# Performance work log

Hardware: AMD Instinct MI355X
Metric: run time of the kernel (lower is better)

## Reference

```python
import jax, jax.numpy as jnp
import numpy as np

N, C_IN, T, V = 64, 64, 256, 25
S = 3            # num_subsets
C_OUT = 128
GROUPS = 8
EPS = 1e-5


def setup_inputs() -> dict:
    key = jax.random.key(0)
    ks = jax.random.split(key, 6)
    x = jax.random.normal(ks[0], (N, C_IN, T, V), dtype=jnp.float32)
    A = jax.random.uniform(ks[1], (S, V, V), dtype=jnp.float32) / V  # normalized-ish adjacency buffer
    PA = jax.random.normal(ks[2], (S, V, V), dtype=jnp.float32) * 0.01  # learnable adjacency offset
    cin_g = C_IN // GROUPS  # 8 input channels per group
    Wg = jax.random.normal(ks[3], (C_OUT * S, cin_g), dtype=jnp.float32) * (1.0 / np.sqrt(cin_g))
    bg = jax.random.normal(ks[4], (C_OUT * S,), dtype=jnp.float32) * 0.01
    gamma = jnp.ones((C_OUT,), dtype=jnp.float32)
    beta = jnp.zeros((C_OUT,), dtype=jnp.float32)
    return {"x": x, "A": A, "PA": PA, "Wg": Wg, "bg": bg, "gamma": gamma, "beta": beta}


def reference(x, A, PA, Wg, bg, gamma, beta):
    n, c, t, v = x.shape
    cin_g = c // GROUPS
    cout_total = Wg.shape[0]          # C_OUT * S
    cout_g = cout_total // GROUPS
    # grouped 1x1 conv: conv_group
    xg = x.reshape(n, GROUPS, cin_g, t, v)
    Wg_ = Wg.reshape(GROUPS, cout_g, cin_g)
    out = jnp.einsum('ngctv,gdc->ngdtv', xg, Wg_).reshape(n, cout_total, t, v)
    out = out + bg[None, :, None, None]
    # split into subsets and apply per-subset adjacency, accumulate
    outs = out.reshape(n, S, cout_total // S, t, v)   # (N,S,Cout,T,V)
    Aeff = A + PA                                      # (S,V,V)
    total = jnp.einsum('nsctv,svw->nctw', outs, Aeff)  # (N,Cout,T,V)
    # BatchNorm2d (training-mode batch statistics, biased variance)
    mean = total.mean(axis=(0, 2, 3), keepdims=True)
    var = ((total - mean) ** 2).mean(axis=(0, 2, 3), keepdims=True)
    y = (total - mean) * jax.lax.rsqrt(var + EPS)
    return y * gamma[None, :, None, None] + beta[None, :, None, None]
```

## Files before the change

kernel.cpp:

```cpp
#include <hip/hip_runtime.h>
#include <math.h>

#define NB   64
#define CIN  64
#define TDIM 256
#define VV   25
#define SS   3
#define COUT 128
#define NTV  (NB * TDIM * VV)
#define OUT_TOTAL (NB * COUT * TDIM * VV)
#define TT   8
#define NTILE (TDIM / TT)

#define WS_STATS 0
#define WS_AE2   2048
#define WS_W2    4160
#define WS_BIAS  7232
#define WS_SCALE 10816
#define WS_SHIFT 10944
#define MID_OFF  16384

__device__ __forceinline__ void fma4(float4& a, float s, const float4& b) {
    a.x = fmaf(s, b.x, a.x);
    a.y = fmaf(s, b.y, a.y);
    a.z = fmaf(s, b.z, a.z);
    a.w = fmaf(s, b.w, a.w);
}

__global__ void prep_kernel(const float* __restrict__ A, const float* __restrict__ PA,
                            const float* __restrict__ Wg, const float* __restrict__ bg,
                            float* __restrict__ ws) {
    const int tid = threadIdx.x;
    for (int i = tid; i < 2048; i += 256) ws[WS_STATS + i] = 0.0f;
    for (int i = tid; i < 25 * 84; i += 256) {
        int v = i / 84, r = i % 84;
        int s = r / 28, w = r % 28;
        float val = 0.0f;
        if (w < 25) {
            int idx = s * 625 + v * 25 + w;
            val = A[idx] + PA[idx];
        }
        ws[WS_AE2 + i] = val;
    }
    for (int i = tid; i < 24 * 128; i += 256) {
        int row = i / 128, c = i % 128;
        int s = row / 8, j = row % 8;
        ws[WS_W2 + i] = Wg[(s * 128 + c) * 8 + j];
    }
    for (int i = tid; i < 128 * 28; i += 256) {
        int c = i / 28, w = i % 28;
        float val = 0.0f;
        if (w < 25) {
            for (int s = 0; s < 3; ++s) {
                float cs = 0.0f;
                for (int v = 0; v < 25; ++v) {
                    int idx = s * 625 + v * 25 + w;
                    cs += A[idx] + PA[idx];
                }
                val += bg[s * 128 + c] * cs;
            }
        }
        ws[WS_BIAS + i] = val;
    }
}

template <bool PERM>
__global__ __launch_bounds__(256, 2)
void main_kernel(const float* __restrict__ x, float* __restrict__ ws,
                 float* __restrict__ out, float* __restrict__ mid) {
    __shared__ __align__(16) float s_x[25 * 68];
    __shared__ __align__(16) float s_ae[25 * 84];
    __shared__ __align__(16) float s_w[24 * 128];
    __shared__ __align__(16) float s_y[3 * 64 * 28];
    __shared__ __align__(16) float s_res[128 * 25];
    __shared__ float s_stats[256];

    const int tid = threadIdx.x;
    const int bid = blockIdx.x;
    const int xcd   = bid & 7;
    const int j     = bid >> 3;
    const int ttile = xcd * 4 + (j & 3);
    const int n     = j >> 2;
    const int t0    = ttile * TT;

    s_stats[tid] = 0.0f;
    for (int i = tid; i < 25 * 84; i += 256) s_ae[i] = ws[WS_AE2 + i];
    for (int i = tid; i < 24 * 128; i += 256) s_w[i] = ws[WS_W2 + i];

    const bool active = tid < 224;
    int c0 = 0, w0 = 0;
    float4 b0 = {0,0,0,0}, b1 = b0, b2 = b0, b3 = b0;
    if (active) {
        int ct = tid & 31, wt = tid >> 5;
        c0 = ct * 4;
        w0 = wt * 4;
        b0 = *(const float4*)&ws[WS_BIAS + (c0 + 0) * 28 + w0];
        b1 = *(const float4*)&ws[WS_BIAS + (c0 + 1) * 28 + w0];
        b2 = *(const float4*)&ws[WS_BIAS + (c0 + 2) * 28 + w0];
        b3 = *(const float4*)&ws[WS_BIAS + (c0 + 3) * 28 + w0];
    }
    float st1[4] = {0, 0, 0, 0};
    float st2[4] = {0, 0, 0, 0};

    const float* xbase = x + (size_t)n * (CIN * TDIM * VV);
    float* obase = out + (size_t)n * (COUT * TDIM * VV);
    float* mbase = mid + ((size_t)n * NTILE + ttile) * (TT * COUT * VV);

    {
        const float* xb = xbase + (size_t)t0 * VV;
        for (int i = tid; i < 64 * 25; i += 256) {
            int cin = i / 25, v = i % 25;
            s_x[v * 68 + cin] = xb[cin * (TDIM * VV) + v];
        }
    }
    __syncthreads();

    for (int task = tid; task < 336; task += 256) {
        int cint = task & 15, swt = task >> 4;
        int cin0 = cint * 4, sw0 = swt * 4;
        float4 a0 = {0, 0, 0, 0}, a1 = a0, a2 = a0, a3 = a0;
        #pragma unroll
        for (int v = 0; v < 25; ++v) {
            float4 xv = *(const float4*)&s_x[v * 68 + cin0];
            float4 av = *(const float4*)&s_ae[v * 84 + sw0];
            fma4(a0, xv.x, av);
            fma4(a1, xv.y, av);
            fma4(a2, xv.z, av);
            fma4(a3, xv.w, av);
        }
        int s = sw0 / 28, w = sw0 % 28;
        int yb = (s * 64 + cin0) * 28 + w;
        *(float4*)&s_y[yb]      = a0;
        *(float4*)&s_y[yb + 28] = a1;
        *(float4*)&s_y[yb + 56] = a2;
        *(float4*)&s_y[yb + 84] = a3;
    }
    __syncthreads();

    for (int tt = 0; tt < TT; ++tt) {
        float xr[7];
        if (tt < TT - 1) {
            const float* xb = xbase + (size_t)(t0 + tt + 1) * VV;
            #pragma unroll
            for (int m = 0; m < 7; ++m) {
                int i = tid + 256 * m;
                if (i < 1600) {
                    int cin = i / 25, v = i - cin * 25;
                    xr[m] = xb[cin * (TDIM * VV) + v];
                }
            }
        }

        if (active) {
            float4 r0 = b0, r1 = b1, r2 = b2, r3 = b3;
            #pragma unroll
            for (int s = 0; s < 3; ++s) {
                int g = (s * 128 + c0) / 48;
                int yb = (s * 64 + g * 8) * 28 + w0;
                int wb = s * 8 * 128 + c0;
                #pragma unroll
                for (int jj = 0; jj < 8; ++jj) {
                    float4 wv = *(const float4*)&s_w[wb + jj * 128];
                    float4 yv = *(const float4*)&s_y[yb + jj * 28];
                    fma4(r0, wv.x, yv);
                    fma4(r1, wv.y, yv);
                    fma4(r2, wv.z, yv);
                    fma4(r3, wv.w, yv);
                }
            }
            float4 rr[4] = {r0, r1, r2, r3};
            #pragma unroll
            for (int a = 0; a < 4; ++a) {
                float4 v = rr[a];
                if (w0 + 3 < 25) {
                    st1[a] += v.x + v.y + v.z + v.w;
                    st2[a] += v.x * v.x + v.y * v.y + v.z * v.z + v.w * v.w;
                } else {
                    st1[a] += v.x;
                    st2[a] += v.x * v.x;
                }
            }
            #pragma unroll
            for (int a = 0; a < 4; ++a) {
                int base = (c0 + a) * 25 + w0;
                s_res[base] = rr[a].x;
                if (w0 + 3 < 25) {
                    s_res[base + 1] = rr[a].y;
                    s_res[base + 2] = rr[a].z;
                    s_res[base + 3] = rr[a].w;
                }
            }
        }

        if (tt < TT - 1) {
            #pragma unroll
            for (int m = 0; m < 7; ++m) {
                int i = tid + 256 * m;
                if (i < 1600) {
                    int cin = i / 25, v = i - cin * 25;
                    s_x[v * 68 + cin] = xr[m];
                }
            }
        }
        __syncthreads();

        if (PERM) {
            float4* mb = (float4*)(mbase + tt * (COUT * VV));
            const float4* sr = (const float4*)s_res;
            for (int i = tid; i < 128 * 25 / 4; i += 256) mb[i] = sr[i];
        } else {
            float* ob = obase + (size_t)(t0 + tt) * VV;
            for (int i = tid; i < 128 * 25; i += 256) {
                int c = i / 25, w = i % 25;
                ob[c * (TDIM * VV) + w] = s_res[i];
            }
        }

        if (tt < TT - 1) {
            for (int task = tid; task < 336; task += 256) {
                int cint = task & 15, swt = task >> 4;
                int cin0 = cint * 4, sw0 = swt * 4;
                float4 a0 = {0, 0, 0, 0}, a1 = a0, a2 = a0, a3 = a0;
                #pragma unroll
                for (int v = 0; v < 25; ++v) {
                    float4 xv = *(const float4*)&s_x[v * 68 + cin0];
                    float4 av = *(const float4*)&s_ae[v * 84 + sw0];
                    fma4(a0, xv.x, av);
                    fma4(a1, xv.y, av);
                    fma4(a2, xv.z, av);
                    fma4(a3, xv.w, av);
                }
                int s = sw0 / 28, w = sw0 % 28;
                int yb = (s * 64 + cin0) * 28 + w;
                *(float4*)&s_y[yb]      = a0;
                *(float4*)&s_y[yb + 28] = a1;
                *(float4*)&s_y[yb + 56] = a2;
                *(float4*)&s_y[yb + 84] = a3;
            }
        }
        __syncthreads();
    }

    if (active) {
        #pragma unroll
        for (int a = 0; a < 4; ++a) {
            atomicAdd(&s_stats[c0 + a], st1[a]);
            atomicAdd(&s_stats[128 + c0 + a], st2[a]);
        }
    }
    __syncthreads();
    if (tid < 128) {
        float* st = ws + WS_STATS + xcd * 256;
        atomicAdd(&st[tid], s_stats[tid]);
        atomicAdd(&st[128 + tid], s_stats[128 + tid]);
    }
}

__global__ void finalize_kernel(const float* __restrict__ gamma,
                                const float* __restrict__ beta,
                                float* __restrict__ ws) {
    const int c = threadIdx.x;
    if (c < 128) {
        float s = 0.0f, q = 0.0f;
        for (int k = 0; k < 8; ++k) {
            s += ws[WS_STATS + k * 256 + c];
            q += ws[WS_STATS + k * 256 + 128 + c];
        }
        const float inv = 1.0f / (float)NTV;
        float mean = s * inv;
        float var = q * inv - mean * mean;
        float sc = gamma[c] * rsqrtf(var + 1e-5f);
        ws[WS_SCALE + c] = sc;
        ws[WS_SHIFT + c] = beta[c] - mean * sc;
    }
}

__global__ __launch_bounds__(256)
void norm_perm(const float* __restrict__ mid, float* __restrict__ out,
               const float* __restrict__ ws) {
    const int bid = blockIdx.x;
    const int n = bid >> 7;
    const int c = bid & 127;
    const float sc = ws[WS_SCALE + c];
    const float sh = ws[WS_SHIFT + c];
    float* ob = out + ((size_t)n * COUT + c) * (TDIM * VV);
    const float* mb = mid + (size_t)n * (TDIM * COUT * VV) + c * VV;
    const int tid = threadIdx.x;
    #pragma unroll
    for (int k = 0; k < 25; ++k) {
        int i = k * 256 + tid;
        int t = i / 25, v = i - t * 25;
        float val = mb[(size_t)t * (COUT * VV) + v];
        ob[i] = fmaf(val, sc, sh);
    }
}

__global__ __launch_bounds__(256)
void norm_inplace(float* __restrict__ out, const float* __restrict__ ws) {
    const int total4 = OUT_TOTAL / 4;
    const int stride = gridDim.x * blockDim.x;
    for (int i = blockIdx.x * blockDim.x + threadIdx.x; i < total4; i += stride) {
        int c = (i / 1600) & 127;
        float sc = ws[WS_SCALE + c];
        float sh = ws[WS_SHIFT + c];
        float4 v = ((float4*)out)[i];
        v.x = fmaf(v.x, sc, sh);
        v.y = fmaf(v.y, sc, sh);
        v.z = fmaf(v.z, sc, sh);
        v.w = fmaf(v.w, sc, sh);
        ((float4*)out)[i] = v;
    }
}

extern "C" void kernel_launch(void* const* d_in, const int* in_sizes, int n_in,
                              void* d_out, int out_size, void* d_ws, size_t ws_size,
                              hipStream_t stream) {
    const float* x     = (const float*)d_in[0];
    const float* A     = (const float*)d_in[1];
    const float* PA    = (const float*)d_in[2];
    const float* Wg    = (const float*)d_in[3];
    const float* bg    = (const float*)d_in[4];
    const float* gamma = (const float*)d_in[5];
    const float* beta  = (const float*)d_in[6];
    float* out = (float*)d_out;
    float* ws  = (float*)d_ws;
    float* mid = ws + MID_OFF;

    const bool perm = ws_size >= ((size_t)MID_OFF + (size_t)OUT_TOTAL) * sizeof(float);

    prep_kernel<<<1, 256, 0, stream>>>(A, PA, Wg, bg, ws);
    if (perm) {
        main_kernel<true><<<NB * NTILE, 256, 0, stream>>>(x, ws, out, mid);
        finalize_kernel<<<1, 128, 0, stream>>>(gamma, beta, ws);
        norm_perm<<<NB * COUT, 256, 0, stream>>>(mid, out, ws);
    } else {
        main_kernel<false><<<NB * NTILE, 256, 0, stream>>>(x, ws, out, mid);
        finalize_kernel<<<1, 128, 0, stream>>>(gamma, beta, ws);
        norm_inplace<<<4096, 256, 0, stream>>>(out, ws);
    }
}
```

Baseline: 1.091 ms.

## Write main-kernel results directly to global and tile norm_perm via shared memory

The main kernel drops its shared-memory result staging buffer and one barrier per time step, storing each thread's 4x4 output tile straight to the intermediate buffer (or to the output), and raises the occupancy hint from 2 to 3 blocks per CU. The norm/permute kernel now has each block handle four channels: it loads contiguous float4 chunks of the intermediate into shared memory, then writes float4 output rows. The aim is fewer barriers, less LDS use and better-coalesced global traffic. The direct stores from the main kernel are less coalesced and partly scalar, and the higher occupancy target may limit registers.

```diff
diff --git a/kernel.cpp b/kernel.cpp
--- a/kernel.cpp
+++ b/kernel.cpp
@@ -65,14 +65,13 @@
 }
 
 template <bool PERM>
-__global__ __launch_bounds__(256, 2)
+__global__ __launch_bounds__(256, 3)
 void main_kernel(const float* __restrict__ x, float* __restrict__ ws,
                  float* __restrict__ out, float* __restrict__ mid) {
     __shared__ __align__(16) float s_x[25 * 68];
     __shared__ __align__(16) float s_ae[25 * 84];
     __shared__ __align__(16) float s_w[24 * 128];
     __shared__ __align__(16) float s_y[3 * 64 * 28];
-    __shared__ __align__(16) float s_res[128 * 25];
     __shared__ float s_stats[256];
 
     const int tid = threadIdx.x;
@@ -172,7 +171,7 @@
             #pragma unroll
             for (int a = 0; a < 4; ++a) {
                 float4 v = rr[a];
-                if (w0 + 3 < 25) {
+                if (w0 < 24) {
                     st1[a] += v.x + v.y + v.z + v.w;
                     st2[a] += v.x * v.x + v.y * v.y + v.z * v.z + v.w * v.w;
                 } else {
@@ -180,14 +179,30 @@
                     st2[a] += v.x * v.x;
                 }
             }
-            #pragma unroll
-            for (int a = 0; a < 4; ++a) {
-                int base = (c0 + a) * 25 + w0;
-                s_res[base] = rr[a].x;
-                if (w0 + 3 < 25) {
-                    s_res[base + 1] = rr[a].y;
-                    s_res[base + 2] = rr[a].z;
-                    s_res[base + 3] = rr[a].w;
+            if (PERM) {
+                float* mt = mbase + tt * (COUT * VV);
+                if (w0 < 24) {
+                    *(float4*)&mt[(c0 + 0) * 25 + w0] = r0;
+                    *(float2*)&mt[(c0 + 2) * 25 + w0]     = make_float2(r2.x, r2.y);
+                    *(float2*)&mt[(c0 + 2) * 25 + w0 + 2] = make_float2(r2.z, r2.w);
+                    float* m1 = &mt[(c0 + 1) * 25 + w0];
+                    m1[0] = r1.x; m1[1] = r1.y; m1[2] = r1.z; m1[3] = r1.w;
+                    float* m3 = &mt[(c0 + 3) * 25 + w0];
+                    m3[0] = r3.x; m3[1] = r3.y; m3[2] = r3.z; m3[3] = r3.w;
+                } else {
+                    mt[(c0 + 0) * 25 + 24] = r0.x;
+                    mt[(c0 + 1) * 25 + 24] = r1.x;
+                    mt[(c0 + 2) * 25 + 24] = r2.x;
+                    mt[(c0 + 3) * 25 + 24] = r3.x;
+                }
+            } else {
+                float* ob = obase + (size_t)(t0 + tt) * VV;
+                #pragma unroll
+                for (int a = 0; a < 4; ++a) {
+                    float4 v = rr[a];
+                    float* row = ob + (size_t)(c0 + a) * (TDIM * VV) + w0;
+                    row[0] = v.x;
+                    if (w0 < 24) { row[1] = v.y; row[2] = v.z; row[3] = v.w; }
                 }
             }
         }
@@ -201,22 +216,8 @@
                     s_x[v * 68 + cin] = xr[m];
                 }
             }
-        }
-        __syncthreads();
-
-        if (PERM) {
-            float4* mb = (float4*)(mbase + tt * (COUT * VV));
-            const float4* sr = (const float4*)s_res;
-            for (int i = tid; i < 128 * 25 / 4; i += 256) mb[i] = sr[i];
-        } else {
-            float* ob = obase + (size_t)(t0 + tt) * VV;
-            for (int i = tid; i < 128 * 25; i += 256) {
-                int c = i / 25, w = i % 25;
-                ob[c * (TDIM * VV) + w] = s_res[i];
-            }
-        }
-
-        if (tt < TT - 1) {
+            __syncthreads();
+
             for (int task = tid; task < 336; task += 256) {
                 int cint = task & 15, swt = task >> 4;
                 int cin0 = cint * 4, sw0 = swt * 4;
@@ -237,8 +238,8 @@
                 *(float4*)&s_y[yb + 56] = a2;
                 *(float4*)&s_y[yb + 84] = a3;
             }
-        }
-        __syncthreads();
+            __syncthreads();
+        }
     }
 
     if (active) {
@@ -278,20 +279,66 @@
 __global__ __launch_bounds__(256)
 void norm_perm(const float* __restrict__ mid, float* __restrict__ out,
                const float* __restrict__ ws) {
+    __shared__ __align__(16) float sb[6400];
+    const int tid = threadIdx.x;
     const int bid = blockIdx.x;
-    const int n = bid >> 7;
-    const int c = bid & 127;
-    const float sc = ws[WS_SCALE + c];
-    const float sh = ws[WS_SHIFT + c];
-    float* ob = out + ((size_t)n * COUT + c) * (TDIM * VV);
-    const float* mb = mid + (size_t)n * (TDIM * COUT * VV) + c * VV;
-    const int tid = threadIdx.x;
+    const int n  = bid >> 5;
+    const int cq = bid & 31;
+    const int c0 = cq * 4;
+
+    float sca[4], sha[4];
     #pragma unroll
-    for (int k = 0; k < 25; ++k) {
-        int i = k * 256 + tid;
-        int t = i / 25, v = i - t * 25;
-        float val = mb[(size_t)t * (COUT * VV) + v];
-        ob[i] = fmaf(val, sc, sh);
+    for (int cl = 0; cl < 4; ++cl) {
+        sca[cl] = ws[WS_SCALE + c0 + cl];
+        sha[cl] = ws[WS_SHIFT + c0 + cl];
+    }
+
+    const float* mb = mid + (size_t)n * (TDIM * COUT * VV) + c0 * VV;
+    for (int tc = 0; tc < 4; ++tc) {
+        const float* mc = mb + (size_t)tc * 64 * (COUT * VV);
+        #pragma unroll
+        for (int k = 0; k < 7; ++k) {
+            int idx = k * 256 + tid;
+            if (idx < 1600) {
+                int t = idx / 25;
+                int q = idx - t * 25;
+                float4 v = *(const float4*)&mc[(size_t)t * (COUT * VV) + q * 4];
+                *(float4*)&sb[idx * 4] = v;
+            }
+        }
+        __syncthreads();
+        #pragma unroll
+        for (int cl = 0; cl < 4; ++cl) {
+            float4* ob4 = (float4*)(out + ((size_t)(n * COUT + c0 + cl)) * (TDIM * VV)
+                                        + tc * 1600);
+            const float sc = sca[cl], sh = sha[cl];
+            #pragma unroll
+            for (int k = 0; k < 2; ++k) {
+                int j4 = k * 256 + tid;
+                if (j4 < 400) {
+                    int jb = j4 * 4;
+                    float4 r;
+                    {
+                        int t = (jb + 0) / 25, v = (jb + 0) - t * 25;
+                        r.x = fmaf(sb[t * 100 + cl * 25 + v], sc, sh);
+                    }
+                    {
+                        int t = (jb + 1) / 25, v = (jb + 1) - t * 25;
+                        r.y = fmaf(sb[t * 100 + cl * 25 + v], sc, sh);
+                    }
+                    {
+                        int t = (jb + 2) / 25, v = (jb + 2) - t * 25;
+                        r.z = fmaf(sb[t * 100 + cl * 25 + v], sc, sh);
+                    }
+                    {
+                        int t = (jb + 3) / 25, v = (jb + 3) - t * 25;
+                        r.w = fmaf(sb[t * 100 + cl * 25 + v], sc, sh);
+                    }
+                    ob4[j4] = r;
+                }
+            }
+        }
+        __syncthreads();
     }
 }
 
@@ -332,7 +379,7 @@
     if (perm) {
         main_kernel<true><<<NB * NTILE, 256, 0, stream>>>(x, ws, out, mid);
         finalize_kernel<<<1, 128, 0, stream>>>(gamma, beta, ws);
-        norm_perm<<<NB * COUT, 256, 0, stream>>>(mid, out, ws);
+        norm_perm<<<NB * 32, 256, 0, stream>>>(mid, out, ws);
     } else {
         main_kernel<false><<<NB * NTILE, 256, 0, stream>>>(x, ws, out, mid);
         finalize_kernel<<<1, 128, 0, stream>>>(gamma, beta, ws);
```

New measurement: 1.565 ms. +43.5%, slower.
